# Performance work log

Hardware: AMD Instinct MI355X
Metric: run time of the kernel (lower is better)

The kernel has to match this reference:

```python
import jax, jax.numpy as jnp
import numpy as np

E = 16          # num_experts
D_FULL = 1024   # full_feature_dim
DM = 128        # expert_dim
S = D_FULL // E # per-expert feature slice = 64
P = 2048        # num patches
B = 8
C = 256
W = 3           # local_window (neighbor experts)
DEPTH = 8       # cantor_depth
NEG = -1e9


def _cantor_coord(pos, max_len, depth):
    x = pos / max(1, max_len - 1)
    x = max(1e-6, min(x, 1.0 - 1e-6))
    val, factor = 0.0, 0.5
    for _ in range(depth):
        x *= 3.0
        d = int(x)
        x -= d
        if d == 2:
            val += factor
        factor *= 0.5
    return val


def _expert_routes():
    coords = np.array([_cantor_coord(i, E, DEPTH) for i in range(E)], dtype=np.float32)
    return np.stack([np.argsort(np.abs(coords - coords[i]), kind='stable')[:W] for i in range(E)]).astype(np.int32)


ROUTES = _expert_routes()  # [E, W] static routing table


def setup_inputs():
    key = jax.random.key(0)
    ks = jax.random.split(key, 8)
    h = S // 4
    lim = float(np.sqrt(6.0 / (S + DM)))  # xavier_uniform bound
    penta = jax.random.normal(ks[5], (E, 5, DM), jnp.float32) * 0.02
    penta = penta / jnp.linalg.norm(penta, axis=-1, keepdims=True)
    return {
        'tokens': jax.random.normal(ks[0], (B, P, D_FULL), jnp.float32),
        'fingerprints': jax.random.uniform(ks[1], (P,), jnp.float32),
        'alpha': jnp.ones((E,), jnp.float32),
        'gate_w1': jax.random.normal(ks[2], (E, S, h), jnp.float32) * 0.05,
        'gate_b1': jnp.zeros((E, h), jnp.float32),
        'gate_w2': jax.random.normal(ks[3], (E, h, 1), jnp.float32) * 0.05,
        'gate_b2': jnp.zeros((E, 1), jnp.float32),
        'q_w': jax.random.uniform(ks[4], (E, S, DM), jnp.float32, -lim, lim),
        'k_w': jax.random.uniform(ks[6], (E, S, DM), jnp.float32, -lim, lim),
        'v_w': jax.random.uniform(ks[7], (E, S, DM), jnp.float32, -lim, lim),
        'penta': penta,
        'fusion_w': jnp.ones((5,), jnp.float32) / 5.0,
        'temperature': jnp.float32(0.5),
    }


def _dispatch(fingerprints):
    # Fingerprint band masks, then fixed-capacity gather (static shapes for jit).
    masks = []
    for e in range(E):
        lo, hi = e / E, (e + 1) / E
        m = (fingerprints >= lo) & ((fingerprints <= hi) if e == E - 1 else (fingerprints < hi))
        masks.append(m)
    masks = jnp.stack(masks)                             # [E, P]
    order = jnp.argsort(jnp.where(masks, 0, 1), axis=1)  # stable: assigned patches first
    idx = order[:, :C]                                   # [E, C]
    valid = jnp.take_along_axis(masks, idx, axis=1)      # [E, C]
    return idx, valid


def _forward(tokens, fingerprints, alpha, gate_w1, gate_b1, gate_w2, gate_b2,
             q_w, k_w, v_w, penta, fusion_w, temperature):
    idx, valid = _dispatch(fingerprints)
    Kaff, Qaff, Vs = [], [], []
    for e in range(E):  # fixed structural loop over experts
        feats = tokens[:, idx[e], e * S:(e + 1) * S]                       # [B, C, S]
        g = jax.nn.sigmoid(jax.nn.gelu(feats @ gate_w1[e] + gate_b1[e]) @ gate_w2[e] + gate_b2[e])
        aw = jax.nn.sigmoid(alpha[e])
        feats = feats * (g * aw + (1.0 - aw))                              # gated features
        Q = feats @ q_w[e]
        K = feats @ k_w[e]
        V = feats @ v_w[e]                                                 # [B, C, DM]
        dirs = penta[e] / jnp.linalg.norm(penta[e], axis=-1, keepdims=True)  # [5, DM]
        Kaff.append(jnp.einsum('bcd,vd->vbc', K, dirs))
        Qaff.append(jnp.einsum('bcd,vd->vbc', Q, dirs))
        Vs.append(V)
    Kaff = jnp.stack(Kaff)   # [E, 5, B, C]
    Qaff = jnp.stack(Qaff)   # [E, 5, B, C]
    Vs = jnp.stack(Vs)       # [E, B, C, DM]
    wdir = jax.nn.softmax(fusion_w)
    vmask = valid.astype(jnp.float32)
    out = jnp.zeros((B, P, DM), jnp.float32)
    for e in range(E):
        nb = ROUTES[e]                                  # static [W]
        Knb, Vnb, vnb = Kaff[nb], Vs[nb], vmask[nb]     # [W,5,B,C], [W,B,C,DM], [W,C]
        scores = jnp.einsum('vbi,nvbj->vbinj', Qaff[e], Knb) / temperature
        scores = jnp.where(vnb[None, None, None, :, :] > 0, scores, NEG)
        attn = jax.nn.softmax(scores.reshape(5, B, C, W * C), axis=-1).reshape(5, B, C, W, C)
        att = jnp.einsum('vbinj,nbjd->vbid', attn, Vnb)  # per-direction attended values
        out_e = jnp.einsum('v,vbid->bid', wdir, att) * vmask[e][None, :, None]
        out = out.at[:, idx[e]].add(out_e)              # scatter back to patch positions
    return out


def reference(tokens, fingerprints, alpha, gate_w1, gate_b1, gate_w2, gate_b2,
              q_w, k_w, v_w, penta, fusion_w, temperature):
    return _forward(tokens, fingerprints, alpha, gate_w1, gate_b1, gate_w2, gate_b2,
                    q_w, k_w, v_w, penta, fusion_w, temperature)
```

## Files before the change

### kernel.cpp

```cpp
#include <hip/hip_runtime.h>
#include <cfloat>
#include <math.h>

#define E 16
#define DFULL 1024
#define DM 128
#define S 64
#define P 2048
#define B 8
#define C 256
#define W 3
#define H 16
#define RQ 16
#define NCH 16
#define RQ2 16
#define NCH2 16
#define LOG2E 1.4426950408889634f
#define WST 272
#define SFT 68

typedef __attribute__((ext_vector_type(8))) short short8;
typedef __attribute__((ext_vector_type(4))) short short4v;
typedef __attribute__((ext_vector_type(4))) float f32x4;
#define MFMA_BF16(a, b, c) __builtin_amdgcn_mfma_f32_16x16x32_bf16((a), (b), (c), 0, 0, 0)

#if defined(__HIP_DEVICE_COMPILE__) && __has_builtin(__builtin_amdgcn_exp2f)
#define EXP2(x) __builtin_amdgcn_exp2f(x)
#else
#define EXP2(x) exp2f(x)
#endif

struct RoutesArg { int nb[E][W]; };

static void compute_routes(int r[E][W]) {
  float coords[E];
  for (int i = 0; i < E; ++i) {
    double x = (double)i / (double)(E - 1);
    if (x < 1e-06) x = 1e-06;
    if (x > 1.0 - 1e-06) x = 1.0 - 1e-06;
    double val = 0.0, factor = 0.5;
    for (int k = 0; k < 8; ++k) {
      x *= 3.0;
      int d = (int)x;
      x -= (double)d;
      if (d == 2) val += factor;
      factor *= 0.5;
    }
    coords[i] = (float)val;
  }
  for (int e = 0; e < E; ++e) {
    float de[E];
    for (int i = 0; i < E; ++i) de[i] = fabsf(coords[i] - coords[e]);
    bool used[E] = {false};
    for (int w = 0; w < W; ++w) {
      int best = -1; float bd = FLT_MAX;
      for (int i = 0; i < E; ++i)
        if (!used[i] && de[i] < bd) { bd = de[i]; best = i; }
      used[best] = true;
      r[e][w] = best;
    }
  }
}

__device__ __forceinline__ unsigned short bfhi(float x) {
  return (unsigned short)(__float_as_uint(x) >> 16);
}
__device__ __forceinline__ float bf2f(unsigned short h) {
  return __uint_as_float(((unsigned)h) << 16);
}
__device__ __forceinline__ float gelu_tanh(float x) {
  float u = 0.7978845608028654f * (x + 0.044715f * x * x * x);
  float ez = __expf(2.0f * u);
  float th = 1.0f - __fdividef(2.0f, ez + 1.0f);
  return 0.5f * x * (1.0f + th);
}
__device__ __forceinline__ float sigmoidf_(float x) {
  return __fdividef(1.0f, 1.0f + __expf(-x));
}

__global__ __launch_bounds__(256) void k_setup(
    const float* __restrict__ fp, const float* __restrict__ qw,
    const float* __restrict__ kw, const float* __restrict__ penta,
    const float* __restrict__ temp, const float* __restrict__ vw,
    int* __restrict__ idx, int* __restrict__ counts,
    unsigned short* __restrict__ qkdT_h, unsigned short* __restrict__ qkdT_l,
    unsigned short* __restrict__ vwT_h, unsigned short* __restrict__ vwT_l) {
  int e = blockIdx.x, t = threadIdx.x;
  __shared__ float s_tr[DM * 65];
  if (blockIdx.y == 1) {
    const float* vwe = vw + (size_t)e * S * DM;
    for (int u = t; u < S * DM; u += 256) {
      int s = u >> 7, d = u & 127;
      s_tr[d * 65 + s] = vwe[u];
    }
    __syncthreads();
    for (int u = t; u < S * DM; u += 256) {
      int d = u >> 6, s = u & 63;
      float f = s_tr[d * 65 + s];
      unsigned short h = bfhi(f), l = bfhi(f - bf2f(h));
      vwT_h[(size_t)e * 8192 + u] = h;
      vwT_l[(size_t)e * 8192 + u] = l;
    }
    return;
  }
  {
    float lo = (float)e * 0.0625f, hi = (float)(e + 1) * 0.0625f;
    bool last = (e == E - 1);
    int p0 = t * 8;
    int m[8]; int ls = 0;
    #pragma unroll
    for (int k = 0; k < 8; ++k) {
      float f = fp[p0 + k];
      bool mm = (f >= lo) && (last ? (f <= hi) : (f < hi));
      m[k] = mm ? 1 : 0;
      ls += m[k];
    }
    __shared__ int sc[256];
    sc[t] = ls;
    __syncthreads();
    for (int o = 1; o < 256; o <<= 1) {
      int v = (t >= o) ? sc[t - o] : 0;
      __syncthreads();
      sc[t] += v;
      __syncthreads();
    }
    int incl = sc[t];
    int M = sc[255];
    int r = incl - ls;
    #pragma unroll
    for (int k = 0; k < 8; ++k) {
      if (m[k]) {
        if (r < C) idx[e * C + r] = p0 + k;
        r++;
      }
    }
    if (t == 0) counts[e] = (M < C) ? M : C;
  }
  __syncthreads();
  __shared__ float s_rn[5];
  if (t < 5) {
    const float* pv = penta + (e * 5 + t) * DM;
    float ss = 0.f;
    for (int d = 0; d < DM; ++d) ss += pv[d] * pv[d];
    s_rn[t] = 1.0f / sqrtf(ss);
  }
  __syncthreads();
  float invT = 1.0f / temp[0];
  int s = t & 63, cg = t >> 6;
  for (int c = cg; c < 10; c += 4) {
    int v = c % 5;
    bool isq = (c < 5);
    const float* wrow = (isq ? qw : kw) + ((size_t)e * S + s) * DM;
    const float* pv = penta + (e * 5 + v) * DM;
    float acc = 0.f;
    #pragma unroll
    for (int d4 = 0; d4 < DM / 4; ++d4) {
      float4 a = ((const float4*)wrow)[d4];
      float4 p = ((const float4*)pv)[d4];
      acc += a.x * p.x + a.y * p.y + a.z * p.z + a.w * p.w;
    }
    float val = acc * s_rn[v] * (isq ? invT : 1.0f);
    unsigned short h = bfhi(val), l = bfhi(val - bf2f(h));
    qkdT_h[(e * 16 + c) * 64 + s] = h;
    qkdT_l[(e * 16 + c) * 64 + s] = l;
  }
  for (int c = 10 + cg; c < 16; c += 4) {
    qkdT_h[(e * 16 + c) * 64 + s] = 0;
    qkdT_l[(e * 16 + c) * 64 + s] = 0;
  }
}

__global__ __launch_bounds__(512, 8) void k_p1(
    const float* __restrict__ tokens, const float* __restrict__ alpha,
    const float* __restrict__ gw1, const float* __restrict__ gb1,
    const float* __restrict__ gw2, const float* __restrict__ gb2,
    const unsigned short* __restrict__ qkdT_h, const unsigned short* __restrict__ qkdT_l,
    const unsigned short* __restrict__ vwT_h, const unsigned short* __restrict__ vwT_l,
    const int* __restrict__ idx, const int* __restrict__ counts,
    float* __restrict__ Qa, float* __restrict__ Ka,
    unsigned short* __restrict__ Vt_h, unsigned short* __restrict__ Vt_l,
    float* __restrict__ kmx, float* __restrict__ kmn,
    float* __restrict__ out) {
  int e = blockIdx.x, b = blockIdx.y, rq = blockIdx.z;
  int t = threadIdx.x;

  {
    int blk = (e * B + b) * NCH + rq;
    if (t < 256) {
      float4 z4 = {0.f, 0.f, 0.f, 0.f};
      ((float4*)out)[(size_t)blk * 256 + t] = z4;
    }
  }

  int Me = counts[e];
  int r0 = rq * RQ;
  if (r0 >= Me) {
    if (t < 5) {
      kmx[((e * 5 + t) * B + b) * NCH + rq] = -FLT_MAX;
      kmn[((e * 5 + t) * B + b) * NCH + rq] = FLT_MAX;
    }
    return;
  }

  __shared__ __align__(16) float s_f[RQ * SFT];
  __shared__ __align__(16) unsigned short s_fh[RQ * 72];
  __shared__ __align__(16) unsigned short s_fl[RQ * 72];
  __shared__ __align__(16) float s_gw1[S * H];
  __shared__ float s_scl[RQ];
  __shared__ float s_kx[5 * RQ], s_kn[5 * RQ];
  __shared__ __align__(16) unsigned short s_vth[DM * 16];
  __shared__ __align__(16) unsigned short s_vtl[DM * 16];

  if (t < 256) {
    int row = t >> 4, q4 = t & 15;
    int ii = r0 + row;
    int pos = (ii < Me) ? idx[e * C + ii] : idx[e * C];
    const float* trow = tokens + ((size_t)b * P + pos) * DFULL + e * S;
    *(float4*)(s_f + row * SFT + q4 * 4) = ((const float4*)trow)[q4];
  } else {
    int u = t - 256;
    ((float4*)s_gw1)[u] = ((const float4*)(gw1 + (size_t)e * S * H))[u];
  }
  __syncthreads();

  if (t < 256) {
    int row = t >> 4, s0 = (t & 15) * 4;
    float4 f4 = *(const float4*)(s_f + row * SFT + s0);
    float fv[4] = {f4.x, f4.y, f4.z, f4.w};
    short4v h4, l4;
    #pragma unroll
    for (int k = 0; k < 4; ++k) {
      unsigned short h = bfhi(fv[k]), l = bfhi(fv[k] - bf2f(h));
      h4[k] = (short)h;
      l4[k] = (short)l;
    }
    *(short4v*)(s_fh + row * 72 + s0) = h4;
    *(short4v*)(s_fl + row * 72 + s0) = l4;
  } else {
    int u = t - 256;
    int row = u >> 4, j = u & 15;
    float hj = gb1[e * H + j];
    #pragma unroll
    for (int s4 = 0; s4 < 16; ++s4) {
      float4 f4 = *(const float4*)(s_f + row * SFT + s4 * 4);
      hj = fmaf(f4.x, s_gw1[(s4 * 4 + 0) * H + j], hj);
      hj = fmaf(f4.y, s_gw1[(s4 * 4 + 1) * H + j], hj);
      hj = fmaf(f4.z, s_gw1[(s4 * 4 + 2) * H + j], hj);
      hj = fmaf(f4.w, s_gw1[(s4 * 4 + 3) * H + j], hj);
    }
    float gz = gelu_tanh(hj) * gw2[e * H + j];
    #pragma unroll
    for (int off = 1; off < 16; off <<= 1) gz += __shfl_xor(gz, off);
    if (j == 0) {
      float aw = sigmoidf_(alpha[e]);
      s_scl[row] = sigmoidf_(gb2[e] + gz) * aw + (1.0f - aw);
    }
  }
  __syncthreads();

  int L = t & 63, wv = t >> 6, quad = L >> 4, col = L & 15;

  {
    const unsigned short* vTh = vwT_h + (size_t)e * 8192;
    const unsigned short* vTl = vwT_l + (size_t)e * 8192;
    f32x4 va = {0.f, 0.f, 0.f, 0.f};
    int d0 = wv * 16 + col;
    #pragma unroll
    for (int kc = 0; kc < 2; ++kc) {
      int ko = kc * 32 + quad * 8;
      short8 ah = *(const short8*)(s_fh + col * 72 + ko);
      short8 al = *(const short8*)(s_fl + col * 72 + ko);
      short8 bh = *(const short8*)(vTh + d0 * 64 + ko);
      short8 bl = *(const short8*)(vTl + d0 * 64 + ko);
      va = MFMA_BF16(ah, bh, va);
      va = MFMA_BF16(ah, bl, va);
      va = MFMA_BF16(al, bh, va);
    }
    #pragma unroll
    for (int reg = 0; reg < 4; ++reg) {
      int row = quad * 4 + reg;
      float f0 = va[reg] * s_scl[row];
      unsigned short h0 = bfhi(f0), l0 = bfhi(f0 - bf2f(h0));
      s_vth[d0 * 16 + row] = h0;
      s_vtl[d0 * 16 + row] = l0;
    }
  }

  if (wv == 0) {
    const unsigned short* qTh = qkdT_h + e * 16 * 64;
    const unsigned short* qTl = qkdT_l + e * 16 * 64;
    f32x4 qa = {0.f, 0.f, 0.f, 0.f};
    #pragma unroll
    for (int kc = 0; kc < 2; ++kc) {
      int ko = kc * 32 + quad * 8;
      short8 ah = *(const short8*)(s_fh + col * 72 + ko);
      short8 al = *(const short8*)(s_fl + col * 72 + ko);
      short8 bh = *(const short8*)(qTh + col * 64 + ko);
      short8 bl = *(const short8*)(qTl + col * 64 + ko);
      qa = MFMA_BF16(ah, bh, qa);
      qa = MFMA_BF16(ah, bl, qa);
      qa = MFMA_BF16(al, bh, qa);
    }
    #pragma unroll
    for (int reg = 0; reg < 4; ++reg) {
      int row = quad * 4 + reg;
      int ii = r0 + row;
      float val = qa[reg] * s_scl[row];
      if (col < 5) {
        if (ii < Me) Qa[((e * 5 + col) * B + b) * C + ii] = val;
      } else if (col < 10) {
        int v = col - 5;
        if (ii < Me) Ka[((e * 5 + v) * B + b) * C + ii] = val;
        s_kx[v * RQ + row] = (ii < Me) ? val : -FLT_MAX;
        s_kn[v * RQ + row] = (ii < Me) ? val : FLT_MAX;
      }
    }
  }
  __syncthreads();
  if (t < 5) {
    float mx = -FLT_MAX, mn = FLT_MAX;
    for (int r = 0; r < RQ; ++r) {
      mx = fmaxf(mx, s_kx[t * RQ + r]);
      mn = fminf(mn, s_kn[t * RQ + r]);
    }
    kmx[((e * 5 + t) * B + b) * NCH + rq] = mx;
    kmn[((e * 5 + t) * B + b) * NCH + rq] = mn;
  }
  if (t < 256) {
    size_t base = (size_t)(e * B + b) * (DM * C);
    int jsl = t >> 7, d = t & 127;
    size_t dst = base + ((size_t)(rq * 2 + jsl) * DM + d) * 8;
    int src = d * 16 + jsl * 8;
    *(short8*)(Vt_h + dst) = *(const short8*)(s_vth + src);
    *(short8*)(Vt_l + dst) = *(const short8*)(s_vtl + src);
  }
}

__global__ __launch_bounds__(512, 8) void k_p2v(
    const float* __restrict__ Qa, const float* __restrict__ Ka,
    const unsigned short* __restrict__ Vt_h, const unsigned short* __restrict__ Vt_l,
    const float* __restrict__ kmx, const float* __restrict__ kmn,
    const int* __restrict__ idx, const int* __restrict__ counts,
    const float* __restrict__ fusw, float* __restrict__ out, RoutesArg R) {
  int e = blockIdx.x, b = blockIdx.y, rq = blockIdx.z;
  int t = threadIdx.x;
  int Me = counts[e];
  int r0 = rq * RQ2;
  if (r0 >= Me) return;

  __shared__ __align__(16) float s_ka[3 * 5 * C];
  __shared__ __align__(16) unsigned short s_wh[RQ2 * WST];
  __shared__ __align__(16) unsigned short s_wl[RQ2 * WST];
  __shared__ float s_l[5 * RQ2];
  __shared__ float s_KX[5], s_KN[5];
  float* s_lp = (float*)s_wh;

  int nbs[3] = {R.nb[e][0], R.nb[e][1], R.nb[e][2]};
  int Mns[3] = {counts[nbs[0]], counts[nbs[1]], counts[nbs[2]]};
  int row = t & 15, jq = t >> 4;
  int ii = r0 + row;
  int L = t & 63, wv = t >> 6, quad = L >> 4, col = L & 15;

  float qv[5];
  #pragma unroll
  for (int v = 0; v < 5; ++v)
    qv[v] = Qa[(((size_t)e * 5 + v) * B + b) * C + ii];
  float fw[5];
  #pragma unroll
  for (int v = 0; v < 5; ++v) fw[v] = fusw[v];

  for (int u = t; u < 960; u += 512) {
    int n = (u >= 640) ? 2 : ((u >= 320) ? 1 : 0);
    int r2 = u - n * 320;
    int v = r2 >> 6, off = r2 & 63;
    ((float4*)s_ka)[n * 320 + (v << 6) + off] =
        ((const float4*)(Ka + (((size_t)nbs[n] * 5 + v) * B + b) * C))[off];
  }
  if (wv < 5) {
    float KX = -FLT_MAX, KN = FLT_MAX;
    if (L < 48) {
      int n = L >> 4, k = L & 15;
      int base = ((nbs[n] * 5 + wv) * B + b) * NCH + k;
      KX = kmx[base];
      KN = kmn[base];
    }
    #pragma unroll
    for (int off = 32; off; off >>= 1) {
      KX = fmaxf(KX, __shfl_xor(KX, off));
      KN = fminf(KN, __shfl_xor(KN, off));
    }
    if (L == 0) { s_KX[wv] = KX; s_KN[wv] = KN; }
  }
  __syncthreads();

  float q2[5], m2[5];
  #pragma unroll
  for (int v = 0; v < 5; ++v) {
    q2[v] = qv[v] * LOG2E;
    m2[v] = ((qv[v] > 0.f) ? qv[v] * s_KX[v] : qv[v] * s_KN[v]) * LOG2E;
  }

  float lp[5] = {0.f, 0.f, 0.f, 0.f, 0.f};
  for (int n = 0; n < 3; ++n) {
    const float* ka_n = s_ka + n * 1280;
    int Mn = Mns[n];
    for (int j = jq; j < Mn; j += 32) {
      #pragma unroll
      for (int v = 0; v < 5; ++v)
        lp[v] += EXP2(fmaf(q2[v], ka_n[v * C + j], -m2[v]));
    }
  }
  #pragma unroll
  for (int v = 0; v < 5; ++v) {
    lp[v] += __shfl_xor(lp[v], 16);
    lp[v] += __shfl_xor(lp[v], 32);
  }
  if (L < 16) {
    #pragma unroll
    for (int v = 0; v < 5; ++v) s_lp[(wv * 5 + v) * RQ2 + L] = lp[v];
  }
  __syncthreads();
  if (t < 80) {
    int v = t >> 4, rw = t & 15;
    float l = 0.f;
    #pragma unroll
    for (int w = 0; w < 8; ++w) l += s_lp[(w * 5 + v) * RQ2 + rw];
    s_l[v * RQ2 + rw] = l;
  }
  __syncthreads();

  float fmx = fw[0];
  #pragma unroll
  for (int v = 1; v < 5; ++v) fmx = fmaxf(fmx, fw[v]);
  float fsum = 0.f;
  #pragma unroll
  for (int v = 0; v < 5; ++v) { fw[v] = __expf(fw[v] - fmx); fsum += fw[v]; }
  float rfs = __fdividef(1.0f, fsum);
  float c2[5];
  #pragma unroll
  for (int v = 0; v < 5; ++v) {
    float cl = __fdividef(fw[v] * rfs, s_l[v * RQ2 + row]);
    c2[v] = __log2f(cl) - m2[v];
  }

  int d0 = wv * 16 + col;
  f32x4 acc = {0.f, 0.f, 0.f, 0.f};

  for (int n = 0; n < 3; ++n) {
    int ne = nbs[n], Mn = Mns[n];
    int kcN = (Mn + 31) >> 5;
    const float* ka_n = s_ka + n * 1280;
    __syncthreads();
    const unsigned short* vbh = Vt_h + (size_t)(ne * B + b) * (DM * C);
    const unsigned short* vbl = Vt_l + (size_t)(ne * B + b) * (DM * C);
    size_t sb0 = ((size_t)quad * DM + d0) * 8;
    short8 bh = *(const short8*)(vbh + sb0);
    short8 bl = *(const short8*)(vbl + sb0);
    int jlim = kcN * 32;
    for (int j0 = jq * 4; j0 < jlim; j0 += 128) {
      short4v h4, l4;
      #pragma unroll
      for (int k2 = 0; k2 < 4; ++k2) {
        int jj = j0 + k2;
        float ww = 0.f;
        if (jj < Mn) {
          #pragma unroll
          for (int v = 0; v < 5; ++v)
            ww += EXP2(fmaf(q2[v], ka_n[v * C + jj], c2[v]));
        }
        unsigned short h = bfhi(ww), l = bfhi(ww - bf2f(h));
        h4[k2] = (short)h;
        l4[k2] = (short)l;
      }
      *(short4v*)(s_wh + row * WST + j0) = h4;
      *(short4v*)(s_wl + row * WST + j0) = l4;
    }
    __syncthreads();
    __builtin_amdgcn_s_setprio(1);
    for (int kc = 0; kc < kcN; ++kc) {
      int kn = (kc + 1 < kcN) ? (kc + 1) : kc;
      size_t sb = ((size_t)(kn * 4 + quad) * DM + d0) * 8;
      short8 nbh = *(const short8*)(vbh + sb);
      short8 nbl = *(const short8*)(vbl + sb);
      int ko = kc * 32 + quad * 8;
      short8 ah = *(const short8*)(s_wh + col * WST + ko);
      short8 al = *(const short8*)(s_wl + col * WST + ko);
      acc = MFMA_BF16(ah, bh, acc);
      acc = MFMA_BF16(ah, bl, acc);
      acc = MFMA_BF16(al, bh, acc);
      bh = nbh;
      bl = nbl;
    }
    __builtin_amdgcn_s_setprio(0);
  }

  #pragma unroll
  for (int reg = 0; reg < 4; ++reg) {
    int rr = quad * 4 + reg;
    int iw = r0 + rr;
    if (iw < Me) {
      int pos = idx[e * C + iw];
      out[((size_t)b * P + pos) * DM + d0] = acc[reg];
    }
  }
}

extern "C" void kernel_launch(void* const* d_in, const int* in_sizes, int n_in,
                              void* d_out, int out_size, void* d_ws, size_t ws_size,
                              hipStream_t stream) {
  const float* tokens = (const float*)d_in[0];
  const float* fingerprints = (const float*)d_in[1];
  const float* alpha = (const float*)d_in[2];
  const float* gw1 = (const float*)d_in[3];
  const float* gb1 = (const float*)d_in[4];
  const float* gw2 = (const float*)d_in[5];
  const float* gb2 = (const float*)d_in[6];
  const float* qw = (const float*)d_in[7];
  const float* kw = (const float*)d_in[8];
  const float* vw = (const float*)d_in[9];
  const float* penta = (const float*)d_in[10];
  const float* fusw = (const float*)d_in[11];
  const float* temp = (const float*)d_in[12];
  float* out = (float*)d_out;

  float* ws = (float*)d_ws;
  float* Qa = ws;
  float* Ka = Qa + (size_t)E * 5 * B * C;
  float* kmx = Ka + (size_t)E * 5 * B * C;
  float* kmn = kmx + (size_t)E * 5 * B * NCH;
  unsigned short* qkdT_h = (unsigned short*)(kmn + (size_t)E * 5 * B * NCH);
  unsigned short* qkdT_l = qkdT_h + (size_t)E * 16 * 64;
  unsigned short* vwT_h = qkdT_l + (size_t)E * 16 * 64;
  unsigned short* vwT_l = vwT_h + (size_t)E * S * DM;
  unsigned short* Vt_h = vwT_l + (size_t)E * S * DM;
  unsigned short* Vt_l = Vt_h + (size_t)E * B * DM * C;
  int* idx = (int*)(Vt_l + (size_t)E * B * DM * C);
  int* counts = idx + (size_t)E * C;

  RoutesArg R;
  compute_routes(R.nb);

  k_setup<<<dim3(E, 2), dim3(256), 0, stream>>>(fingerprints, qw, kw, penta, temp, vw,
                                                idx, counts, qkdT_h, qkdT_l, vwT_h, vwT_l);
  k_p1<<<dim3(E, B, NCH), dim3(512), 0, stream>>>(tokens, alpha, gw1, gb1, gw2, gb2,
                                                  qkdT_h, qkdT_l, vwT_h, vwT_l,
                                                  idx, counts, Qa, Ka, Vt_h, Vt_l,
                                                  kmx, kmn, out);
  k_p2v<<<dim3(E, B, NCH2), dim3(512), 0, stream>>>(Qa, Ka, Vt_h, Vt_l, kmx, kmn,
                                                    idx, counts, fusw, out, R);
}
```

Before: 169.9 us.

## Double-buffer weight tiles and preload V fragments across neighbor experts in p2v

Restructures the k_p2v neighbor loop into a software pipeline. The shared weight buffers are doubled, so computing the exp weights for neighbor n+1 can overlap with the MFMA accumulation for neighbor n. The first four V chunks of the next neighbor are preloaded into registers ahead of time, which cuts the number of __syncthreads per neighbor. The cost is more LDS and more registers, and launch bounds are lowered from 8 to 4 waves per EU to make room, which reduces occupancy.

```diff
diff --git a/kernel.cpp b/kernel.cpp
--- a/kernel.cpp
+++ b/kernel.cpp
@@ -336,7 +336,7 @@
   }
 }
 
-__global__ __launch_bounds__(512, 8) void k_p2v(
+__global__ __launch_bounds__(512, 4) void k_p2v(
     const float* __restrict__ Qa, const float* __restrict__ Ka,
     const unsigned short* __restrict__ Vt_h, const unsigned short* __restrict__ Vt_l,
     const float* __restrict__ kmx, const float* __restrict__ kmn,
@@ -349,8 +349,8 @@
   if (r0 >= Me) return;
 
   __shared__ __align__(16) float s_ka[3 * 5 * C];
-  __shared__ __align__(16) unsigned short s_wh[RQ2 * WST];
-  __shared__ __align__(16) unsigned short s_wl[RQ2 * WST];
+  __shared__ __align__(16) unsigned short s_wh[2 * RQ2 * WST];
+  __shared__ __align__(16) unsigned short s_wl[2 * RQ2 * WST];
   __shared__ float s_l[5 * RQ2];
   __shared__ float s_KX[5], s_KN[5];
   float* s_lp = (float*)s_wh;
@@ -446,53 +446,138 @@
   int d0 = wv * 16 + col;
   f32x4 acc = {0.f, 0.f, 0.f, 0.f};
 
-  for (int n = 0; n < 3; ++n) {
-    int ne = nbs[n], Mn = Mns[n];
-    int kcN = (Mn + 31) >> 5;
-    const float* ka_n = s_ka + n * 1280;
-    __syncthreads();
-    const unsigned short* vbh = Vt_h + (size_t)(ne * B + b) * (DM * C);
-    const unsigned short* vbl = Vt_l + (size_t)(ne * B + b) * (DM * C);
-    size_t sb0 = ((size_t)quad * DM + d0) * 8;
-    short8 bh = *(const short8*)(vbh + sb0);
-    short8 bl = *(const short8*)(vbl + sb0);
-    int jlim = kcN * 32;
-    for (int j0 = jq * 4; j0 < jlim; j0 += 128) {
-      short4v h4, l4;
-      #pragma unroll
-      for (int k2 = 0; k2 < 4; ++k2) {
-        int jj = j0 + k2;
-        float ww = 0.f;
-        if (jj < Mn) {
-          #pragma unroll
-          for (int v = 0; v < 5; ++v)
-            ww += EXP2(fmaf(q2[v], ka_n[v * C + jj], c2[v]));
-        }
-        unsigned short h = bfhi(ww), l = bfhi(ww - bf2f(h));
-        h4[k2] = (short)h;
-        l4[k2] = (short)l;
-      }
-      *(short4v*)(s_wh + row * WST + j0) = h4;
-      *(short4v*)(s_wl + row * WST + j0) = l4;
-    }
-    __syncthreads();
-    __builtin_amdgcn_s_setprio(1);
-    for (int kc = 0; kc < kcN; ++kc) {
-      int kn = (kc + 1 < kcN) ? (kc + 1) : kc;
-      size_t sb = ((size_t)(kn * 4 + quad) * DM + d0) * 8;
-      short8 nbh = *(const short8*)(vbh + sb);
-      short8 nbl = *(const short8*)(vbl + sb);
-      int ko = kc * 32 + quad * 8;
-      short8 ah = *(const short8*)(s_wh + col * WST + ko);
-      short8 al = *(const short8*)(s_wl + col * WST + ko);
-      acc = MFMA_BF16(ah, bh, acc);
-      acc = MFMA_BF16(ah, bl, acc);
-      acc = MFMA_BF16(al, bh, acc);
-      bh = nbh;
-      bl = nbl;
-    }
-    __builtin_amdgcn_s_setprio(0);
-  }
+  short8 fAh0 = {}, fAl0 = {}, fAh1 = {}, fAl1 = {};
+  short8 fAh2 = {}, fAl2 = {}, fAh3 = {}, fAl3 = {};
+  short8 fBh0 = {}, fBl0 = {}, fBh1 = {}, fBl1 = {};
+  short8 fBh2 = {}, fBl2 = {}, fBh3 = {}, fBl3 = {};
+
+#define PRELOAD(N, H0, L0, H1, L1, H2, L2, H3, L3)                            \
+  {                                                                           \
+    int ne_ = nbs[N];                                                         \
+    int kcN_ = (Mns[N] + 31) >> 5;                                            \
+    const unsigned short* vbh_ = Vt_h + (size_t)(ne_ * B + b) * (DM * C);     \
+    const unsigned short* vbl_ = Vt_l + (size_t)(ne_ * B + b) * (DM * C);     \
+    size_t sb_ = ((size_t)quad * DM + d0) * 8;                                \
+    H0 = *(const short8*)(vbh_ + sb_);                                        \
+    L0 = *(const short8*)(vbl_ + sb_);                                        \
+    if (kcN_ > 1) {                                                           \
+      sb_ = ((size_t)(4 + quad) * DM + d0) * 8;                               \
+      H1 = *(const short8*)(vbh_ + sb_);                                      \
+      L1 = *(const short8*)(vbl_ + sb_);                                      \
+    }                                                                         \
+    if (kcN_ > 2) {                                                           \
+      sb_ = ((size_t)(8 + quad) * DM + d0) * 8;                               \
+      H2 = *(const short8*)(vbh_ + sb_);                                      \
+      L2 = *(const short8*)(vbl_ + sb_);                                      \
+    }                                                                         \
+    if (kcN_ > 3) {                                                           \
+      sb_ = ((size_t)(12 + quad) * DM + d0) * 8;                              \
+      H3 = *(const short8*)(vbh_ + sb_);                                      \
+      L3 = *(const short8*)(vbl_ + sb_);                                      \
+    }                                                                         \
+  }
+
+#define PHASE_A(N, PL)                                                        \
+  {                                                                           \
+    int Mn_ = Mns[N];                                                         \
+    const float* ka_ = s_ka + (N) * 1280;                                     \
+    int jlim_ = ((Mn_ + 31) >> 5) * 32;                                       \
+    for (int j0 = jq * 4; j0 < jlim_; j0 += 128) {                            \
+      short4v h4, l4;                                                         \
+      _Pragma("unroll")                                                       \
+      for (int k2 = 0; k2 < 4; ++k2) {                                        \
+        int jj = j0 + k2;                                                     \
+        float ww = 0.f;                                                       \
+        if (jj < Mn_) {                                                       \
+          _Pragma("unroll")                                                   \
+          for (int v = 0; v < 5; ++v)                                         \
+            ww += EXP2(fmaf(q2[v], ka_[v * C + jj], c2[v]));                  \
+        }                                                                     \
+        unsigned short h_ = bfhi(ww), l_ = bfhi(ww - bf2f(h_));               \
+        h4[k2] = (short)h_;                                                   \
+        l4[k2] = (short)l_;                                                   \
+      }                                                                       \
+      *(short4v*)(s_wh + (PL) * (RQ2 * WST) + row * WST + j0) = h4;           \
+      *(short4v*)(s_wl + (PL) * (RQ2 * WST) + row * WST + j0) = l4;           \
+    }                                                                         \
+  }
+
+#define PHASE_B(N, PL, H0, L0, H1, L1, H2, L2, H3, L3)                        \
+  {                                                                           \
+    int kcN_ = (Mns[N] + 31) >> 5;                                            \
+    const unsigned short* swh_ = s_wh + (PL) * (RQ2 * WST);                   \
+    const unsigned short* swl_ = s_wl + (PL) * (RQ2 * WST);                   \
+    {                                                                         \
+      short8 ah = *(const short8*)(swh_ + col * WST + quad * 8);              \
+      short8 al = *(const short8*)(swl_ + col * WST + quad * 8);              \
+      acc = MFMA_BF16(ah, H0, acc);                                           \
+      acc = MFMA_BF16(ah, L0, acc);                                           \
+      acc = MFMA_BF16(al, H0, acc);                                           \
+    }                                                                         \
+    if (kcN_ > 1) {                                                           \
+      short8 ah = *(const short8*)(swh_ + col * WST + 32 + quad * 8);         \
+      short8 al = *(const short8*)(swl_ + col * WST + 32 + quad * 8);         \
+      acc = MFMA_BF16(ah, H1, acc);                                           \
+      acc = MFMA_BF16(ah, L1, acc);                                           \
+      acc = MFMA_BF16(al, H1, acc);                                           \
+    }                                                                         \
+    if (kcN_ > 2) {                                                           \
+      short8 ah = *(const short8*)(swh_ + col * WST + 64 + quad * 8);         \
+      short8 al = *(const short8*)(swl_ + col * WST + 64 + quad * 8);         \
+      acc = MFMA_BF16(ah, H2, acc);                                           \
+      acc = MFMA_BF16(ah, L2, acc);                                           \
+      acc = MFMA_BF16(al, H2, acc);                                           \
+    }                                                                         \
+    if (kcN_ > 3) {                                                           \
+      short8 ah = *(const short8*)(swh_ + col * WST + 96 + quad * 8);         \
+      short8 al = *(const short8*)(swl_ + col * WST + 96 + quad * 8);         \
+      acc = MFMA_BF16(ah, H3, acc);                                           \
+      acc = MFMA_BF16(ah, L3, acc);                                           \
+      acc = MFMA_BF16(al, H3, acc);                                           \
+    }                                                                         \
+    if (kcN_ > 4) {                                                           \
+      int ne_ = nbs[N];                                                       \
+      const unsigned short* vbh_ = Vt_h + (size_t)(ne_ * B + b) * (DM * C);   \
+      const unsigned short* vbl_ = Vt_l + (size_t)(ne_ * B + b) * (DM * C);   \
+      for (int kc = 4; kc < kcN_; ++kc) {                                     \
+        size_t sb = ((size_t)(kc * 4 + quad) * DM + d0) * 8;                  \
+        short8 bh = *(const short8*)(vbh_ + sb);                              \
+        short8 bl = *(const short8*)(vbl_ + sb);                              \
+        int ko = kc * 32 + quad * 8;                                          \
+        short8 ah = *(const short8*)(swh_ + col * WST + ko);                  \
+        short8 al = *(const short8*)(swl_ + col * WST + ko);                  \
+        acc = MFMA_BF16(ah, bh, acc);                                         \
+        acc = MFMA_BF16(ah, bl, acc);                                         \
+        acc = MFMA_BF16(al, bh, acc);                                         \
+      }                                                                       \
+    }                                                                         \
+  }
+
+  PRELOAD(0, fAh0, fAl0, fAh1, fAl1, fAh2, fAl2, fAh3, fAl3)
+  PHASE_A(0, 0)
+  __syncthreads();
+
+  PRELOAD(1, fBh0, fBl0, fBh1, fBl1, fBh2, fBl2, fBh3, fBl3)
+  __builtin_amdgcn_s_setprio(1);
+  PHASE_B(0, 0, fAh0, fAl0, fAh1, fAl1, fAh2, fAl2, fAh3, fAl3)
+  PHASE_A(1, 1)
+  __builtin_amdgcn_s_setprio(0);
+  __syncthreads();
+
+  PRELOAD(2, fAh0, fAl0, fAh1, fAl1, fAh2, fAl2, fAh3, fAl3)
+  __builtin_amdgcn_s_setprio(1);
+  PHASE_B(1, 1, fBh0, fBl0, fBh1, fBl1, fBh2, fBl2, fBh3, fBl3)
+  PHASE_A(2, 0)
+  __builtin_amdgcn_s_setprio(0);
+  __syncthreads();
+
+  __builtin_amdgcn_s_setprio(1);
+  PHASE_B(2, 0, fAh0, fAl0, fAh1, fAl1, fAh2, fAl2, fAh3, fAl3)
+  __builtin_amdgcn_s_setprio(0);
+
+#undef PRELOAD
+#undef PHASE_A
+#undef PHASE_B
 
   #pragma unroll
   for (int reg = 0; reg < 4; ++reg) {
```

Result: no change. 172.6 us (+1.5%).
